# Performance work log

Hardware: AMD Instinct MI355X
Metric: run time of the kernel (lower is better)

Reference implementation:

```python
import jax, jax.numpy as jnp
import numpy as np

# Model dims
B, T, D = 2, 2048, 768
H, DH = 12, 64          # attention heads, head_dim = D // H
IH, ID = 4, 64          # indexer heads, indexer dim
K = 64                  # top_k selected KV tokens per query


def setup_inputs() -> dict:
    key = jax.random.key(0)
    ks = jax.random.split(key, 10)
    s = 0.02
    return {
        "x": jax.random.normal(ks[0], (B, T, D), jnp.float32),
        # lightning indexer projections (nn.Linear weights are [out, in])
        "wq_i": jax.random.normal(ks[1], (IH * ID, D), jnp.float32) * s,
        "bq_i": jnp.zeros((IH * ID,), jnp.float32),
        "wk_i": jax.random.normal(ks[2], (IH * ID, D), jnp.float32) * s,
        "bk_i": jnp.zeros((IH * ID,), jnp.float32),
        "w_head": jax.random.normal(ks[3], (IH,), jnp.float32),
        # fused qkv + out projections
        "w_qkv": jax.random.normal(ks[4], (3 * D, D), jnp.float32) * s,
        "b_qkv": jnp.zeros((3 * D,), jnp.float32),
        "w_out": jax.random.normal(ks[5], (D, D), jnp.float32) * s,
        "b_out": jnp.zeros((D,), jnp.float32),
    }


def reference(x, wq_i, bq_i, wk_i, bk_i, w_head, w_qkv, b_qkv, w_out, b_out):
    Bb, Tt, Dd = x.shape
    # fused QKV: [B,T,3,H,DH]
    qkv = (x @ w_qkv.T + b_qkv).reshape(Bb, Tt, 3, H, DH)
    q, k, v = qkv[:, :, 0], qkv[:, :, 1], qkv[:, :, 2]  # each [B,T,H,DH]

    # lightning indexer: I[b,t,s] = sum_h w_h * relu(qI[b,t,h] . kI[b,s,h])
    qI = (x @ wq_i.T + bq_i).reshape(Bb, Tt, IH, ID)
    kI = (x @ wk_i.T + bk_i).reshape(Bb, Tt, IH, ID)
    rel = jax.nn.relu(jnp.einsum('bthd,bshd->bhts', qI, kI))  # [B,IH,T,T]
    scores = jnp.einsum('h,bhts->bts', w_head, rel)           # [B,T,T]

    # causal mask, then top-k KV selection per query
    causal = jnp.tril(jnp.ones((Tt, Tt), dtype=bool))
    scores = jnp.where(causal[None], scores, -jnp.inf)
    vals, idx = jax.lax.top_k(scores, K)                      # [B,T,K]
    valid = jnp.isfinite(vals)                                # early queries have < K causal keys
    routing = jnp.where(valid, vals, 0.0)                     # routing weights = scores * valid

    # gather selected K/V tokens (shared across attention heads)
    gather = jax.vmap(lambda arr, i: arr[i])                  # per-batch fancy gather
    k_sel = gather(k, idx)                                    # [B,T,K,H,DH]
    v_sel = gather(v, idx)                                    # [B,T,K,H,DH]

    # sparse attention over the K selected tokens
    att = jnp.einsum('bthd,btkhd->bhtk', q, k_sel) / jnp.sqrt(jnp.float32(DH))
    att = jnp.where(valid[:, None], att, -jnp.inf)            # mask invalid slots
    p = jax.nn.softmax(att, axis=-1)                          # [B,H,T,K]
    p = p * routing[:, None]                                  # indexer routing gate
    out = jnp.einsum('bhtk,btkhd->bthd', p, v_sel).reshape(Bb, Tt, Dd)
    return out @ w_out.T + b_out
```

## Files before the change

kernel.cpp:

```cpp
#include <hip/hip_runtime.h>
#include <hip/hip_bf16.h>
#include <math.h>

#define B_   2
#define T_   2048
#define D_   768
#define H_   12
#define DH_  64
#define IH_  4
#define ID_  64
#define K_   64
#define M_   (B_ * T_)
#define NQKV 2304

#define LDT 132

typedef __attribute__((ext_vector_type(8))) short bf16x8;
typedef __attribute__((ext_vector_type(4))) float f32x4;

#define GLOBAL_AS __attribute__((address_space(1)))
#define LDS_AS    __attribute__((address_space(3)))

__device__ __forceinline__ void split2(float f, unsigned short& h, unsigned short& l)
{
    __bf16 b = (__bf16)f;
    h = __builtin_bit_cast(unsigned short, b);
    __bf16 c = (__bf16)(f - (float)b);
    l = __builtin_bit_cast(unsigned short, c);
}

__global__ __launch_bounds__(256) void split_kernel(
    const float* __restrict__ in, unsigned short* __restrict__ hi,
    unsigned short* __restrict__ lo, int n4)
{
    int i = blockIdx.x * 256 + threadIdx.x;
    if (i >= n4) return;
    float4 v = ((const float4*)in)[i];
    ushort4 hv, lv;
    split2(v.x, hv.x, lv.x);
    split2(v.y, hv.y, lv.y);
    split2(v.z, hv.z, lv.z);
    split2(v.w, hv.w, lv.w);
    ((ushort4*)hi)[i] = hv;
    ((ushort4*)lo)[i] = lv;
}

__global__ __launch_bounds__(256) void gemm_bf16split(
    const unsigned short* __restrict__ Ahi, const unsigned short* __restrict__ Alo,
    const unsigned short* __restrict__ Whi, const unsigned short* __restrict__ Wlo,
    const float* __restrict__ bias, float* __restrict__ C, int Nn)
{
    __shared__ char lsa[128 * 128];
    __shared__ char lsb[128 * 128];
    const int tid = threadIdx.x;
    const int lane = tid & 63;
    const int wv = tid >> 6;
    const int bm = blockIdx.y * 128, bn = blockIdx.x * 128;
    const int wr = (wv >> 1) * 64, wc = (wv & 1) * 64;

    f32x4 acc[4][4];
    const f32x4 zero = {0.0f, 0.0f, 0.0f, 0.0f};
#pragma unroll
    for (int m = 0; m < 4; ++m)
#pragma unroll
        for (int n = 0; n < 4; ++n) acc[m][n] = zero;

    const int srow = lane >> 3;
    const int scol = (lane & 7) * 16;

    for (int kt = 0; kt < 36; ++kt) {
        const unsigned short* Ap;
        const unsigned short* Wp;
        int kc;
        if (kt < 12)      { Ap = Ahi; Wp = Whi; kc = kt * 64; }
        else if (kt < 24) { Ap = Ahi; Wp = Wlo; kc = (kt - 12) * 64; }
        else              { Ap = Alo; Wp = Whi; kc = (kt - 24) * 64; }

#pragma unroll
        for (int i = 0; i < 4; ++i) {
            int rl = wv * 32 + i * 8 + srow;
            int sb = scol ^ ((rl & 7) << 4);
            const char* ga = (const char*)Ap + ((size_t)(bm + rl) * D_ + kc) * 2 + sb;
            __builtin_amdgcn_global_load_lds((GLOBAL_AS const void*)ga,
                (LDS_AS void*)(lsa + (wv * 32 + i * 8) * 128), 16, 0, 0);
            const char* gb = (const char*)Wp + ((size_t)(bn + rl) * D_ + kc) * 2 + sb;
            __builtin_amdgcn_global_load_lds((GLOBAL_AS const void*)gb,
                (LDS_AS void*)(lsb + (wv * 32 + i * 8) * 128), 16, 0, 0);
        }
        __syncthreads();

#pragma unroll
        for (int ks = 0; ks < 2; ++ks) {
            bf16x8 afr[4], bfr[4];
            const int kb = ks * 64 + ((lane >> 4) * 16);
#pragma unroll
            for (int m = 0; m < 4; ++m) {
                int r = wr + m * 16 + (lane & 15);
                afr[m] = *(const bf16x8*)(lsa + r * 128 + (kb ^ ((r & 7) << 4)));
                int rn = wc + m * 16 + (lane & 15);
                bfr[m] = *(const bf16x8*)(lsb + rn * 128 + (kb ^ ((rn & 7) << 4)));
            }
#pragma unroll
            for (int m = 0; m < 4; ++m)
#pragma unroll
                for (int n = 0; n < 4; ++n)
                    acc[m][n] = __builtin_amdgcn_mfma_f32_16x16x32_bf16(
                        afr[m], bfr[n], acc[m][n], 0, 0, 0);
        }
        __syncthreads();
    }

    float bv[4];
#pragma unroll
    for (int n = 0; n < 4; ++n) bv[n] = bias[bn + wc + n * 16 + (lane & 15)];
#pragma unroll
    for (int m = 0; m < 4; ++m)
#pragma unroll
        for (int n = 0; n < 4; ++n)
#pragma unroll
            for (int j = 0; j < 4; ++j) {
                int row = bm + wr + m * 16 + (lane >> 4) * 4 + j;
                int col = bn + wc + n * 16 + (lane & 15);
                C[(size_t)row * Nn + col] = acc[m][n][j] + bv[n];
            }
}

__global__ __launch_bounds__(256) void gemm_qiki64(
    const float* __restrict__ x,
    const float* __restrict__ wq, const float* __restrict__ bq,
    const float* __restrict__ wk, const float* __restrict__ bk,
    float* __restrict__ qI, float* __restrict__ kI)
{
    __shared__ float la[32][LDT];
    __shared__ float lb[32][68];
    const int tid = threadIdx.x;
    const int tx = tid & 15, ty = tid >> 4;
    const int bm = blockIdx.y * 128;
    int bn = blockIdx.x * 64;
    const float* W; const float* bias; float* Out;
    if (bn < 256) { W = wq; bias = bq; Out = qI; }
    else          { W = wk; bias = bk; Out = kI; bn -= 256; }

    float acc[8][4];
#pragma unroll
    for (int i = 0; i < 8; ++i)
#pragma unroll
        for (int j = 0; j < 4; ++j) acc[i][j] = 0.0f;

    for (int k0 = 0; k0 < D_; k0 += 32) {
#pragma unroll
        for (int i = 0; i < 4; ++i) {
            int f4 = tid + (i << 8);
            int r = f4 >> 3, cq = f4 & 7;
            float4 a = *(const float4*)(x + (size_t)(bm + r) * D_ + k0 + (cq << 2));
            la[cq * 4 + 0][r] = a.x;
            la[cq * 4 + 1][r] = a.y;
            la[cq * 4 + 2][r] = a.z;
            la[cq * 4 + 3][r] = a.w;
        }
#pragma unroll
        for (int i = 0; i < 2; ++i) {
            int f4 = tid + (i << 8);
            int r = f4 >> 3, cq = f4 & 7;
            float4 w4 = *(const float4*)(W + (size_t)(bn + r) * D_ + k0 + (cq << 2));
            lb[cq * 4 + 0][r] = w4.x;
            lb[cq * 4 + 1][r] = w4.y;
            lb[cq * 4 + 2][r] = w4.z;
            lb[cq * 4 + 3][r] = w4.w;
        }
        __syncthreads();
#pragma unroll
        for (int kk = 0; kk < 32; ++kk) {
            float4 a0 = *(const float4*)&la[kk][ty * 8];
            float4 a1 = *(const float4*)&la[kk][ty * 8 + 4];
            float4 b0 = *(const float4*)&lb[kk][tx * 4];
            float av[8] = {a0.x, a0.y, a0.z, a0.w, a1.x, a1.y, a1.z, a1.w};
            float bv4[4] = {b0.x, b0.y, b0.z, b0.w};
#pragma unroll
            for (int i = 0; i < 8; ++i)
#pragma unroll
                for (int j = 0; j < 4; ++j)
                    acc[i][j] = fmaf(av[i], bv4[j], acc[i][j]);
        }
        __syncthreads();
    }

    float bs[4];
    {
        float4 q0 = *(const float4*)(bias + bn + tx * 4);
        bs[0] = q0.x; bs[1] = q0.y; bs[2] = q0.z; bs[3] = q0.w;
    }
#pragma unroll
    for (int i = 0; i < 8; ++i) {
        int rr = bm + ty * 8 + i;
        float4 o;
        o.x = acc[i][0] + bs[0];
        o.y = acc[i][1] + bs[1];
        o.z = acc[i][2] + bs[2];
        o.w = acc[i][3] + bs[3];
        *(float4*)(Out + (size_t)rr * (IH_ * ID_) + bn + tx * 4) = o;
    }
}

__global__ __launch_bounds__(256) void scores_kernel(
    const float* __restrict__ qI, const float* __restrict__ kI,
    const float* __restrict__ w_head, float* __restrict__ scores)
{
    const int is = blockIdx.x, it = blockIdx.y, b = blockIdx.z;
    if (is > it) return;
    __shared__ float lq[32][LDT];
    __shared__ float lk[32][LDT];
    const int tid = threadIdx.x;
    const int tx = tid & 15, ty = tid >> 4;
    const int t0 = it * 128, s0 = is * 128;

    float sc[8][8];
#pragma unroll
    for (int i = 0; i < 8; ++i)
#pragma unroll
        for (int j = 0; j < 8; ++j) sc[i][j] = 0.0f;

    for (int h = 0; h < IH_; ++h) {
        float rel[8][8];
#pragma unroll
        for (int i = 0; i < 8; ++i)
#pragma unroll
            for (int j = 0; j < 8; ++j) rel[i][j] = 0.0f;

        for (int k0 = 0; k0 < ID_; k0 += 32) {
#pragma unroll
            for (int i = 0; i < 4; ++i) {
                int f4 = tid + (i << 8);
                int r = f4 >> 3;
                int cq = f4 & 7;
                float4 a = *(const float4*)(qI + (size_t)(b * T_ + t0 + r) * (IH_ * ID_) + h * ID_ + k0 + (cq << 2));
                lq[cq * 4 + 0][r] = a.x;
                lq[cq * 4 + 1][r] = a.y;
                lq[cq * 4 + 2][r] = a.z;
                lq[cq * 4 + 3][r] = a.w;
                float4 c = *(const float4*)(kI + (size_t)(b * T_ + s0 + r) * (IH_ * ID_) + h * ID_ + k0 + (cq << 2));
                lk[cq * 4 + 0][r] = c.x;
                lk[cq * 4 + 1][r] = c.y;
                lk[cq * 4 + 2][r] = c.z;
                lk[cq * 4 + 3][r] = c.w;
            }
            __syncthreads();
#pragma unroll
            for (int kk = 0; kk < 32; ++kk) {
                float4 a0 = *(const float4*)&lq[kk][ty * 8];
                float4 a1 = *(const float4*)&lq[kk][ty * 8 + 4];
                float4 b0 = *(const float4*)&lk[kk][tx * 8];
                float4 b1 = *(const float4*)&lk[kk][tx * 8 + 4];
                float av[8] = {a0.x, a0.y, a0.z, a0.w, a1.x, a1.y, a1.z, a1.w};
                float bv[8] = {b0.x, b0.y, b0.z, b0.w, b1.x, b1.y, b1.z, b1.w};
#pragma unroll
                for (int i = 0; i < 8; ++i)
#pragma unroll
                    for (int j = 0; j < 8; ++j)
                        rel[i][j] = fmaf(av[i], bv[j], rel[i][j]);
            }
            __syncthreads();
        }
        float wh = w_head[h];
#pragma unroll
        for (int i = 0; i < 8; ++i)
#pragma unroll
            for (int j = 0; j < 8; ++j)
                sc[i][j] += wh * fmaxf(rel[i][j], 0.0f);
    }

#pragma unroll
    for (int i = 0; i < 8; ++i) {
        int tt = t0 + ty * 8 + i;
        float* sp = scores + ((size_t)b * T_ + tt) * T_ + s0 + tx * 8;
        float4 o0 = {sc[i][0], sc[i][1], sc[i][2], sc[i][3]};
        float4 o1 = {sc[i][4], sc[i][5], sc[i][6], sc[i][7]};
        *(float4*)sp = o0;
        *(float4*)(sp + 4) = o1;
    }
}

__global__ __launch_bounds__(256) void topk_kernel(
    const float* __restrict__ scores, int* __restrict__ idx_out,
    float* __restrict__ rout_out)
{
    const int row = blockIdx.x;
    const int b = row >> 11;
    const int t = row & (T_ - 1);
    const int tid = threadIdx.x;
    const int lane = tid & 63;
    const int wv = tid >> 6;
    const int n = t + 1;
    const float* srow = scores + ((size_t)b * T_ + t) * T_;
    const size_t obase = (size_t)row * K_;

    if (n <= K_) {
        for (int r = tid; r < K_; r += 256) {
            idx_out[obase + r] = (r < n) ? r : 0;
            rout_out[obase + r] = (r < n) ? srow[r] : 0.0f;
        }
        return;
    }

    __shared__ unsigned int keys[T_];
    __shared__ unsigned int hist[256];
    __shared__ unsigned int nb[256];
    __shared__ int wt0[4], wt1[4];
    __shared__ unsigned int sh_prefix;
    __shared__ int sh_need;

    for (int s = tid; s < n; s += 256) {
        unsigned int u = __float_as_uint(srow[s]);
        u ^= (u & 0x80000000u) ? 0xffffffffu : 0x80000000u;
        keys[s] = u;
    }

    unsigned int prefix = 0;
    int need = K_;
    for (int pass = 0; pass < 4; ++pass) {
        const int shift = 24 - pass * 8;
        const unsigned int pmask = (pass == 0) ? 0u : (0xffffffffu << (shift + 8));
        hist[tid] = 0;
        __syncthreads();
        for (int s = tid; s < n; s += 256) {
            unsigned int k = keys[s];
            if ((k & pmask) == prefix)
                atomicAdd(&hist[(k >> shift) & 0xffu], 1u);
        }
        __syncthreads();
        int v = (int)hist[tid];
#pragma unroll
        for (int off = 1; off < 64; off <<= 1) {
            int o = __shfl_down(v, off);
            if (lane + off < 64) v += o;
        }
        if (lane == 0) wt0[wv] = v;
        __syncthreads();
        int wadd = 0;
#pragma unroll
        for (int w2 = 0; w2 < 4; ++w2) if (w2 > wv) wadd += wt0[w2];
        int sfx = v + wadd;
        nb[tid] = (unsigned)sfx;
        __syncthreads();
        int sfx1 = (tid < 255) ? (int)nb[tid + 1] : 0;
        if (sfx >= need && sfx1 < need) {
            sh_prefix = prefix | ((unsigned)tid << shift);
            sh_need = need - sfx1;
        }
        __syncthreads();
        prefix = sh_prefix;
        need = sh_need;
        __syncthreads();
    }
    const unsigned int thr = prefix;

    const int chunk = (n + 255) >> 8;
    const int base = tid * chunk;
    int cg = 0, ce = 0;
    for (int j = 0; j < chunk; ++j) {
        int s = base + j;
        if (s < n) {
            unsigned int k = keys[s];
            cg += (k > thr);
            ce += (k == thr);
        }
    }
    int vg = cg, ve = ce;
#pragma unroll
    for (int off = 1; off < 64; off <<= 1) {
        int og = __shfl_up(vg, off);
        int oe = __shfl_up(ve, off);
        if (lane >= off) { vg += og; ve += oe; }
    }
    if (lane == 63) { wt0[wv] = vg; wt1[wv] = ve; }
    __syncthreads();
    int offg = 0, offe = 0, G = 0;
#pragma unroll
    for (int w2 = 0; w2 < 4; ++w2) {
        G += wt0[w2];
        if (w2 < wv) { offg += wt0[w2]; offe += wt1[w2]; }
    }
    int sg = vg + offg - cg;
    int se = ve + offe - ce;
    for (int j = 0; j < chunk; ++j) {
        int s = base + j;
        if (s < n) {
            unsigned int k = keys[s];
            if (k >= thr) {
                unsigned int u = k ^ ((k & 0x80000000u) ? 0x80000000u : 0xffffffffu);
                if (k > thr) {
                    idx_out[obase + sg] = s;
                    rout_out[obase + sg] = __uint_as_float(u);
                    sg++;
                } else {
                    if (se < need) {
                        idx_out[obase + G + se] = s;
                        rout_out[obase + G + se] = __uint_as_float(u);
                    }
                    se++;
                }
            }
        }
    }
}

__global__ __launch_bounds__(256) void attn_kernel(
    const float* __restrict__ qkv, const int* __restrict__ idx,
    const float* __restrict__ routing,
    unsigned short* __restrict__ atthi, unsigned short* __restrict__ attlo)
{
    const int bid = blockIdx.x;
    const int row = ((bid & 7) << 9) | (bid >> 3);
    const int b = row >> 11;
    const int t = row & (T_ - 1);
    const int tid = threadIdx.x;
    const int lane = tid & 63;
    const int wave = tid >> 6;
    const int nv = (t + 1) < K_ ? (t + 1) : K_;

    __shared__ float qs[D_];
    __shared__ int vboff[K_];
    __shared__ float pbuf[4][3][K_];

    for (int i = tid; i < D_; i += 256) qs[i] = qkv[(size_t)row * NQKV + i];

    int myidx = 0;
    float myrout = 0.0f;
    if (lane < nv) {
        myidx = idx[(size_t)row * K_ + lane];
        myrout = routing[(size_t)row * K_ + lane];
    }
    if (wave == 0) vboff[lane] = (b * T_ + myidx) * NQKV;
    __syncthreads();

    const float scale = 0.125f;
#pragma unroll
    for (int hh = 0; hh < 3; ++hh) {
        const int h = wave + hh * 4;
        float att = -INFINITY;
        if (lane < nv) {
            const float* kp = qkv + (size_t)(b * T_ + myidx) * NQKV + D_ + h * DH_;
            const float* qp = qs + h * DH_;
            float acc = 0.0f;
#pragma unroll
            for (int d4 = 0; d4 < 16; ++d4) {
                float4 kv4 = *(const float4*)(kp + d4 * 4);
                float4 q4 = *(const float4*)(qp + d4 * 4);
                acc = fmaf(kv4.x, q4.x, acc);
                acc = fmaf(kv4.y, q4.y, acc);
                acc = fmaf(kv4.z, q4.z, acc);
                acc = fmaf(kv4.w, q4.w, acc);
            }
            att = acc * scale;
        }
        float m = att;
#pragma unroll
        for (int off = 32; off; off >>= 1) m = fmaxf(m, __shfl_xor(m, off));
        float e = (lane < nv) ? __expf(att - m) : 0.0f;
        float ssum = e;
#pragma unroll
        for (int off = 32; off; off >>= 1) ssum += __shfl_xor(ssum, off);
        pbuf[wave][hh][lane] = e / ssum * myrout;
    }
    __syncthreads();

    const int sub = lane >> 4;
    const int dl = lane & 15;
    float4 a0 = {0, 0, 0, 0}, a1 = {0, 0, 0, 0}, a2 = {0, 0, 0, 0};
    const float* vbase = qkv + 2 * D_ + wave * DH_ + dl * 4;

    if (nv == K_) {
#pragma unroll
        for (int j = 0; j < 16; ++j) {
            const int k = sub * 16 + j;
            float p0 = pbuf[wave][0][k];
            float p1 = pbuf[wave][1][k];
            float p2 = pbuf[wave][2][k];
            const float* vp = vbase + vboff[k];
            float4 v0 = *(const float4*)(vp);
            float4 v1 = *(const float4*)(vp + 4 * DH_);
            float4 v2 = *(const float4*)(vp + 8 * DH_);
            a0.x = fmaf(p0, v0.x, a0.x); a0.y = fmaf(p0, v0.y, a0.y);
            a0.z = fmaf(p0, v0.z, a0.z); a0.w = fmaf(p0, v0.w, a0.w);
            a1.x = fmaf(p1, v1.x, a1.x); a1.y = fmaf(p1, v1.y, a1.y);
            a1.z = fmaf(p1, v1.z, a1.z); a1.w = fmaf(p1, v1.w, a1.w);
            a2.x = fmaf(p2, v2.x, a2.x); a2.y = fmaf(p2, v2.y, a2.y);
            a2.z = fmaf(p2, v2.z, a2.z); a2.w = fmaf(p2, v2.w, a2.w);
        }
    } else {
        int kc = nv - sub * 16;
        kc = kc < 0 ? 0 : (kc > 16 ? 16 : kc);
        for (int j = 0; j < kc; ++j) {
            const int k = sub * 16 + j;
            float p0 = pbuf[wave][0][k];
            float p1 = pbuf[wave][1][k];
            float p2 = pbuf[wave][2][k];
            const float* vp = vbase + vboff[k];
            float4 v0 = *(const float4*)(vp);
            float4 v1 = *(const float4*)(vp + 4 * DH_);
            float4 v2 = *(const float4*)(vp + 8 * DH_);
            a0.x = fmaf(p0, v0.x, a0.x); a0.y = fmaf(p0, v0.y, a0.y);
            a0.z = fmaf(p0, v0.z, a0.z); a0.w = fmaf(p0, v0.w, a0.w);
            a1.x = fmaf(p1, v1.x, a1.x); a1.y = fmaf(p1, v1.y, a1.y);
            a1.z = fmaf(p1, v1.z, a1.z); a1.w = fmaf(p1, v1.w, a1.w);
            a2.x = fmaf(p2, v2.x, a2.x); a2.y = fmaf(p2, v2.y, a2.y);
            a2.z = fmaf(p2, v2.z, a2.z); a2.w = fmaf(p2, v2.w, a2.w);
        }
    }

#pragma unroll
    for (int off = 16; off <= 32; off <<= 1) {
        a0.x += __shfl_xor(a0.x, off); a0.y += __shfl_xor(a0.y, off);
        a0.z += __shfl_xor(a0.z, off); a0.w += __shfl_xor(a0.w, off);
        a1.x += __shfl_xor(a1.x, off); a1.y += __shfl_xor(a1.y, off);
        a1.z += __shfl_xor(a1.z, off); a1.w += __shfl_xor(a1.w, off);
        a2.x += __shfl_xor(a2.x, off); a2.y += __shfl_xor(a2.y, off);
        a2.z += __shfl_xor(a2.z, off); a2.w += __shfl_xor(a2.w, off);
    }

    if (sub == 0) {
        const float accs[3][4] = {{a0.x, a0.y, a0.z, a0.w},
                                  {a1.x, a1.y, a1.z, a1.w},
                                  {a2.x, a2.y, a2.z, a2.w}};
#pragma unroll
        for (int hh = 0; hh < 3; ++hh) {
            const int h = wave + hh * 4;
            ushort4 hv, lv;
            split2(accs[hh][0], hv.x, lv.x);
            split2(accs[hh][1], hv.y, lv.y);
            split2(accs[hh][2], hv.z, lv.z);
            split2(accs[hh][3], hv.w, lv.w);
            const size_t o = ((size_t)row * D_ + h * DH_ + dl * 4) >> 2;
            ((ushort4*)atthi)[o] = hv;
            ((ushort4*)attlo)[o] = lv;
        }
    }
}

extern "C" void kernel_launch(void* const* d_in, const int* in_sizes, int n_in,
                              void* d_out, int out_size, void* d_ws, size_t ws_size,
                              hipStream_t stream)
{
    const float* x      = (const float*)d_in[0];
    const float* wq_i   = (const float*)d_in[1];
    const float* bq_i   = (const float*)d_in[2];
    const float* wk_i   = (const float*)d_in[3];
    const float* bk_i   = (const float*)d_in[4];
    const float* w_head = (const float*)d_in[5];
    const float* w_qkv  = (const float*)d_in[6];
    const float* b_qkv  = (const float*)d_in[7];
    const float* w_out  = (const float*)d_in[8];
    const float* b_out  = (const float*)d_in[9];
    float* out = (float*)d_out;

    char* w = (char*)d_ws;
    float* scoresb        = (float*)w;
    unsigned short* wqh   = (unsigned short*)w;
    unsigned short* wql   = (unsigned short*)(w + 4194304);
    unsigned short* woh   = (unsigned short*)(w + 8388608);
    unsigned short* wol   = (unsigned short*)(w + 12582912);
    float* qkv            = (float*)(w + 33554432);
    float* qI             = (float*)(w + 71303168);
    float* kI             = (float*)(w + 75497472);
    float* routing        = (float*)(w + 79691776);
    int*   idxb           = (int*)  (w + 80740352);
    unsigned short* xhi   = (unsigned short*)(w + 81788928);
    unsigned short* xlo   = (unsigned short*)(w + 88080384);
    unsigned short* atthi = xhi;
    unsigned short* attlo = xlo;

    dim3 blk(256);

    split_kernel<<<dim3((M_ * D_ / 4 + 255) / 256), blk, 0, stream>>>(x, xhi, xlo, M_ * D_ / 4);
    split_kernel<<<dim3((NQKV * D_ / 4 + 255) / 256), blk, 0, stream>>>(w_qkv, wqh, wql, NQKV * D_ / 4);

    gemm_bf16split<<<dim3(NQKV / 128, M_ / 128), blk, 0, stream>>>(xhi, xlo, wqh, wql, b_qkv, qkv, NQKV);

    gemm_qiki64<<<dim3(8, M_ / 128), blk, 0, stream>>>(x, wq_i, bq_i, wk_i, bk_i, qI, kI);

    scores_kernel<<<dim3(T_ / 128, T_ / 128, B_), blk, 0, stream>>>(qI, kI, w_head, scoresb);
    topk_kernel<<<dim3(M_), blk, 0, stream>>>(scoresb, idxb, routing);

    split_kernel<<<dim3((D_ * D_ / 4 + 255) / 256), blk, 0, stream>>>(w_out, woh, wol, D_ * D_ / 4);

    attn_kernel<<<dim3(M_), blk, 0, stream>>>(qkv, idxb, routing, atthi, attlo);

    gemm_bf16split<<<dim3(D_ / 128, M_ / 128), blk, 0, stream>>>(atthi, attlo, woh, wol, b_out, out, D_);
}
```

Measured before the change: 486.9 us.

## Load hi/lo A and W tiles together per K-step to reuse fragments across split products

The split-bf16 GEMM previously made three separate passes over K (hi*hi, hi*lo, lo*hi), each reloading A and W tiles. Now each 32-wide K step loads all four tiles (Ahi, Alo, Whi, Wlo) into LDS at once and issues the three MFMAs per fragment pair from registers. This cuts global and LDS traffic for the repeated hi operands. In exchange the K step is narrower, so there are more barriers per unit of MFMA work, and the swizzle pattern changes.

```diff
diff --git a/kernel.cpp b/kernel.cpp
--- a/kernel.cpp
+++ b/kernel.cpp
@@ -50,8 +50,7 @@
     const unsigned short* __restrict__ Whi, const unsigned short* __restrict__ Wlo,
     const float* __restrict__ bias, float* __restrict__ C, int Nn)
 {
-    __shared__ char lsa[128 * 128];
-    __shared__ char lsb[128 * 128];
+    __shared__ char lds[4][128 * 64];
     const int tid = threadIdx.x;
     const int lane = tid & 63;
     const int wv = tid >> 6;
@@ -65,48 +64,49 @@
 #pragma unroll
         for (int n = 0; n < 4; ++n) acc[m][n] = zero;
 
-    const int srow = lane >> 3;
-    const int scol = (lane & 7) * 16;
-
-    for (int kt = 0; kt < 36; ++kt) {
-        const unsigned short* Ap;
-        const unsigned short* Wp;
-        int kc;
-        if (kt < 12)      { Ap = Ahi; Wp = Whi; kc = kt * 64; }
-        else if (kt < 24) { Ap = Ahi; Wp = Wlo; kc = (kt - 12) * 64; }
-        else              { Ap = Alo; Wp = Whi; kc = (kt - 24) * 64; }
-
-#pragma unroll
-        for (int i = 0; i < 4; ++i) {
-            int rl = wv * 32 + i * 8 + srow;
-            int sb = scol ^ ((rl & 7) << 4);
-            const char* ga = (const char*)Ap + ((size_t)(bm + rl) * D_ + kc) * 2 + sb;
-            __builtin_amdgcn_global_load_lds((GLOBAL_AS const void*)ga,
-                (LDS_AS void*)(lsa + (wv * 32 + i * 8) * 128), 16, 0, 0);
-            const char* gb = (const char*)Wp + ((size_t)(bn + rl) * D_ + kc) * 2 + sb;
-            __builtin_amdgcn_global_load_lds((GLOBAL_AS const void*)gb,
-                (LDS_AS void*)(lsb + (wv * 32 + i * 8) * 128), 16, 0, 0);
-        }
-        __syncthreads();
-
-#pragma unroll
-        for (int ks = 0; ks < 2; ++ks) {
-            bf16x8 afr[4], bfr[4];
-            const int kb = ks * 64 + ((lane >> 4) * 16);
-#pragma unroll
-            for (int m = 0; m < 4; ++m) {
-                int r = wr + m * 16 + (lane & 15);
-                afr[m] = *(const bf16x8*)(lsa + r * 128 + (kb ^ ((r & 7) << 4)));
-                int rn = wc + m * 16 + (lane & 15);
-                bfr[m] = *(const bf16x8*)(lsb + rn * 128 + (kb ^ ((rn & 7) << 4)));
+    const int srow = lane >> 2;
+    const int scol = (lane & 3) * 16;
+
+    for (int kc = 0; kc < D_; kc += 32) {
+#pragma unroll
+        for (int j = 0; j < 8; ++j) {
+            const int buf = j >> 1;
+            const int seg = wv * 2 + (j & 1);
+            const int rl = seg * 16 + srow;
+            const int cb = scol ^ ((rl & 3) << 4);
+            const unsigned short* src = (buf == 0) ? Ahi : (buf == 1) ? Alo
+                                      : (buf == 2) ? Whi : Wlo;
+            const int grow = ((buf < 2) ? bm : bn) + rl;
+            const char* g = (const char*)src + ((size_t)grow * D_ + kc) * 2 + cb;
+            __builtin_amdgcn_global_load_lds((GLOBAL_AS const void*)g,
+                (LDS_AS void*)(lds[buf] + seg * (16 * 64)), 16, 0, 0);
+        }
+        __syncthreads();
+
+        bf16x8 ah[4], al[4], bh[4], bl[4];
+        const int cslot = (lane >> 4) * 16;
+#pragma unroll
+        for (int m = 0; m < 4; ++m) {
+            const int r = wr + m * 16 + (lane & 15);
+            const int co = cslot ^ ((r & 3) << 4);
+            ah[m] = *(const bf16x8*)(lds[0] + r * 64 + co);
+            al[m] = *(const bf16x8*)(lds[1] + r * 64 + co);
+            const int rn = wc + m * 16 + (lane & 15);
+            const int cn = cslot ^ ((rn & 3) << 4);
+            bh[m] = *(const bf16x8*)(lds[2] + rn * 64 + cn);
+            bl[m] = *(const bf16x8*)(lds[3] + rn * 64 + cn);
+        }
+#pragma unroll
+        for (int m = 0; m < 4; ++m)
+#pragma unroll
+            for (int n = 0; n < 4; ++n) {
+                acc[m][n] = __builtin_amdgcn_mfma_f32_16x16x32_bf16(
+                    ah[m], bh[n], acc[m][n], 0, 0, 0);
+                acc[m][n] = __builtin_amdgcn_mfma_f32_16x16x32_bf16(
+                    ah[m], bl[n], acc[m][n], 0, 0, 0);
+                acc[m][n] = __builtin_amdgcn_mfma_f32_16x16x32_bf16(
+                    al[m], bh[n], acc[m][n], 0, 0, 0);
             }
-#pragma unroll
-            for (int m = 0; m < 4; ++m)
-#pragma unroll
-                for (int n = 0; n < 4; ++n)
-                    acc[m][n] = __builtin_amdgcn_mfma_f32_16x16x32_bf16(
-                        afr[m], bfr[n], acc[m][n], 0, 0, 0);
-        }
         __syncthreads();
     }
 
```

Measured after the change: 500.7 us. 1.03x slower.
